# Optimization experiments

Measured on AMD Instinct MI355X. Metric: run time of the kernel, lower is better.

Reference implementation:

```python
import jax, jax.numpy as jnp
import numpy as np

G = 32               # sdf grid resolution (grid_size init default)
SCALE_FACTOR = 0.2   # forward default scale_factor
EPS = 1e-12


def setup_inputs() -> dict:
    key = jax.random.key(0)
    k1, k2 = jax.random.split(key)
    H, V, F = 2, 778, 1538  # two hands, MANO topology
    vertices = jax.random.normal(k1, (H, V, 3), dtype=jnp.float32)
    faces = jax.random.randint(k2, (F, 3), 0, V, dtype=jnp.int32)
    return {"vertices": vertices, "faces": faces}


def _sdiv(n, d):
    return n / jnp.where(jnp.abs(d) < EPS, EPS, d)


def _point_tri_dist2(p, a, b, c):
    # p: [P,1,3]; a,b,c: [1,F,3] -> squared distance [P,F] (Ericson closest-point)
    ab = b - a; ac = c - a; ap = p - a
    d1 = jnp.sum(ab * ap, -1); d2 = jnp.sum(ac * ap, -1)
    bp = p - b; d3 = jnp.sum(ab * bp, -1); d4 = jnp.sum(ac * bp, -1)
    cp = p - c; d5 = jnp.sum(ab * cp, -1); d6 = jnp.sum(ac * cp, -1)
    vc = d1 * d4 - d3 * d2
    vb = d5 * d2 - d1 * d6
    va = d3 * d6 - d5 * d4
    denom = va + vb + vc
    v_in = _sdiv(vb, denom); w_in = _sdiv(vc, denom)
    res = a + ab * v_in[..., None] + ac * w_in[..., None]  # face interior
    # edge BC
    cond = ((va <= 0) & ((d4 - d3) >= 0) & ((d5 - d6) >= 0))[..., None]
    w = _sdiv(d4 - d3, (d4 - d3) + (d5 - d6))[..., None]
    res = jnp.where(cond, b + (c - b) * w, res)
    # edge AC
    cond = ((vb <= 0) & (d2 >= 0) & (d6 <= 0))[..., None]
    w = _sdiv(d2, d2 - d6)[..., None]
    res = jnp.where(cond, a + ac * w, res)
    # edge AB
    cond = ((vc <= 0) & (d1 >= 0) & (d3 <= 0))[..., None]
    w = _sdiv(d1, d1 - d3)[..., None]
    res = jnp.where(cond, a + ab * w, res)
    # vertex regions (highest precedence)
    res = jnp.where(((d6 >= 0) & (d5 <= d6))[..., None], jnp.broadcast_to(c, res.shape), res)
    res = jnp.where(((d3 >= 0) & (d4 <= d3))[..., None], jnp.broadcast_to(b, res.shape), res)
    res = jnp.where(((d1 <= 0) & (d2 <= 0))[..., None], jnp.broadcast_to(a, res.shape), res)
    return jnp.sum((p - res) ** 2, -1)


def _inside(p, a, b, c):
    # parity of +x ray intersections (Moller-Trumbore with dir = (1,0,0))
    e1 = b - a; e2 = c - a
    det = e1[..., 1] * (-e2[..., 2]) + e1[..., 2] * e2[..., 1]  # dot(e1, cross(dir,e2))
    inv = _sdiv(1.0, det)
    s = p - a
    u = (s[..., 1] * (-e2[..., 2]) + s[..., 2] * e2[..., 1]) * inv
    q = jnp.cross(s, e1)
    v = q[..., 0] * inv                # dot(dir, q)
    t = jnp.sum(e2 * q, -1) * inv
    hit = (jnp.abs(det) > 1e-9) & (u >= 0) & (u <= 1) & (v >= 0) & (u + v <= 1) & (t > 0)
    return (jnp.sum(hit.astype(jnp.int32), axis=-1) % 2) == 1


def _sdf_grid(tri):
    # tri: [F,3,3] scaled triangles -> phi [G,G,G] laid out [z,y,x] (grid_sample DHW)
    a = tri[None, :, 0]; b = tri[None, :, 1]; c = tri[None, :, 2]
    lin = jnp.linspace(-1.0, 1.0, G, dtype=tri.dtype)
    zz, yy, xx = jnp.meshgrid(lin, lin, lin, indexing='ij')
    pts = jnp.stack([xx, yy, zz], -1).reshape(G, G * G, 3)  # chunk over z-slabs

    def slab(ps):
        p = ps[:, None, :]
        d2 = jnp.min(_point_tri_dist2(p, a, b, c), axis=1)
        ins = _inside(p, a, b, c)
        return jnp.where(ins, jnp.sqrt(jnp.maximum(d2, 0.0)), 0.0)

    return jax.lax.map(slab, pts).reshape(G, G, G)


def _trilinear(phi, coords):
    # grid_sample(align_corners=True, padding_mode='zeros'), coords [N,3] in xyz order
    g = G - 1
    f = (coords + 1.0) * 0.5 * g
    fx, fy, fz = f[:, 0], f[:, 1], f[:, 2]
    x0f = jnp.floor(fx); y0f = jnp.floor(fy); z0f = jnp.floor(fz)
    wx = fx - x0f; wy = fy - y0f; wz = fz - z0f
    x0 = x0f.astype(jnp.int32); y0 = y0f.astype(jnp.int32); z0 = z0f.astype(jnp.int32)

    def corner(zi, yi, xi, w):
        valid = (zi >= 0) & (zi <= g) & (yi >= 0) & (yi <= g) & (xi >= 0) & (xi <= g)
        val = phi[jnp.clip(zi, 0, g), jnp.clip(yi, 0, g), jnp.clip(xi, 0, g)]
        return jnp.where(valid, val, 0.0) * w

    out = (corner(z0, y0, x0, (1 - wz) * (1 - wy) * (1 - wx))
           + corner(z0, y0, x0 + 1, (1 - wz) * (1 - wy) * wx)
           + corner(z0, y0 + 1, x0, (1 - wz) * wy * (1 - wx))
           + corner(z0, y0 + 1, x0 + 1, (1 - wz) * wy * wx)
           + corner(z0 + 1, y0, x0, wz * (1 - wy) * (1 - wx))
           + corner(z0 + 1, y0, x0 + 1, wz * (1 - wy) * wx)
           + corner(z0 + 1, y0 + 1, x0, wz * wy * (1 - wx))
           + corner(z0 + 1, y0 + 1, x0 + 1, wz * wy * wx))
    return out


def reference(vertices, faces):
    H = vertices.shape[0]
    bmin = vertices.min(axis=1)   # [H,3]
    bmax = vertices.max(axis=1)
    center = jax.lax.stop_gradient(((bmin + bmax) * 0.5)[:, None, :])           # [H,1,3]
    scale = jax.lax.stop_gradient(
        ((1.0 + SCALE_FACTOR) * 0.5 * (bmax - bmin).max(-1))[:, None, None])    # [H,1,1]
    v_scaled = jax.lax.stop_gradient((vertices - center) / scale)
    tris = v_scaled[:, faces]                                                    # [H,F,3,3]
    phi = jax.lax.stop_gradient(jax.vmap(_sdf_grid)(tris))                       # [H,G,G,G]
    i = 1  # hardcoded loop 'for i in [1]' in the source
    coords = ((vertices - center[i][None]) / scale[i][None]).reshape(-1, 3)
    phi_val = _trilinear(phi[i], coords).reshape(H, -1)
    weights = jnp.ones((H, 1), dtype=vertices.dtype).at[i, 0].set(0.0)
    loss = jnp.sum(weights * phi_val) / (H ** 2)
    return loss
```

## Files before the change

kernel.cpp:

```cpp
#include <hip/hip_runtime.h>
#include <math.h>

#define NNODE 32768
#define NTHR  256
#define CH    256
#define MAXC  (CH + 63)

__device__ __forceinline__ float rguard(float d) {
    float dd = (fabsf(d) < 1e-12f) ? 1e-12f : d;
    return __builtin_amdgcn_rcpf(dd);
}

__device__ __forceinline__ void cell_of(float px, float py, float pz,
                                        int& x0, int& y0, int& z0,
                                        float& wx, float& wy, float& wz) {
#pragma clang fp contract(off)
    float fx = (px + 1.0f) * 0.5f * 31.0f;
    float fy = (py + 1.0f) * 0.5f * 31.0f;
    float fz = (pz + 1.0f) * 0.5f * 31.0f;
    float x0f = floorf(fx), y0f = floorf(fy), z0f = floorf(fz);
    wx = fx - x0f; wy = fy - y0f; wz = fz - z0f;
    x0 = (int)fmaxf(fminf(x0f, 33.0f), -2.0f);
    y0 = (int)fmaxf(fminf(y0f, 33.0f), -2.0f);
    z0 = (int)fmaxf(fminf(z0f, 33.0f), -2.0f);
}

__device__ __forceinline__ void bbox_of(const float* __restrict__ verts, int V,
                                        float& ocx, float& ocy, float& ocz,
                                        float& osc) {
#pragma clang fp contract(off)
    const float* v1 = verts + (size_t)V * 3;
    float mn[3] = {1e30f, 1e30f, 1e30f};
    float mx[3] = {-1e30f, -1e30f, -1e30f};
    for (int i = threadIdx.x; i < V; i += blockDim.x) {
        for (int c = 0; c < 3; ++c) {
            float val = v1[i * 3 + c];
            mn[c] = fminf(mn[c], val);
            mx[c] = fmaxf(mx[c], val);
        }
    }
    for (int off = 32; off >= 1; off >>= 1) {
        for (int c = 0; c < 3; ++c) {
            mn[c] = fminf(mn[c], __shfl_down(mn[c], off));
            mx[c] = fmaxf(mx[c], __shfl_down(mx[c], off));
        }
    }
    __shared__ float smn[16][3], smx[16][3];
    int wv = threadIdx.x >> 6, lane = threadIdx.x & 63;
    if (lane == 0)
        for (int c = 0; c < 3; ++c) { smn[wv][c] = mn[c]; smx[wv][c] = mx[c]; }
    __syncthreads();
    const int nw = (int)blockDim.x >> 6;
    float ext = -1e30f, cc[3];
    for (int c = 0; c < 3; ++c) {
        float lo = 1e30f, hi = -1e30f;
        for (int w = 0; w < nw; ++w) {
            lo = fminf(lo, smn[w][c]);
            hi = fmaxf(hi, smx[w][c]);
        }
        cc[c] = (lo + hi) * 0.5f;
        ext = fmaxf(ext, hi - lo);
    }
    ocx = cc[0]; ocy = cc[1]; ocz = cc[2];
    osc = (1.0f + 0.2f) * 0.5f * ext;
    __syncthreads();
}

__device__ __forceinline__ void tri_node(
        float ax, float ay, float az, float abx, float aby, float abz,
        float acx, float acy, float acz, float inv, float det,
        float dbb, float dbc, float dcc,
        float px, float py, float pz, float& mind2, int& h) {
    float apx = px - ax, apy = py - ay, apz = pz - az;
    {
#pragma clang fp contract(fast)
        float d1 = abx * apx + aby * apy + abz * apz;
        float d2 = acx * apx + acy * apy + acz * apz;
        float d3 = d1 - dbb;
        float d4 = d2 - dbc;
        float d5 = d1 - dbc;
        float d6 = d2 - dcc;
        float vc = d1 * d4 - d3 * d2;
        float vb = d5 * d2 - d1 * d6;
        float va = d3 * d6 - d5 * d4;
        float denom = va + vb + vc;
        float rd = rguard(denom);
        float v_in = vb * rd, w_in = vc * rd;
        float rx = ax + abx * v_in + acx * w_in;
        float ry = ay + aby * v_in + acy * w_in;
        float rz = az + abz * v_in + acz * w_in;
        if (va <= 0.0f && (d4 - d3) >= 0.0f && (d5 - d6) >= 0.0f) {
            float w2 = (d4 - d3) * rguard((d4 - d3) + (d5 - d6));
            rx = ax + abx + (acx - abx) * w2;
            ry = ay + aby + (acy - aby) * w2;
            rz = az + abz + (acz - abz) * w2;
        }
        if (vb <= 0.0f && d2 >= 0.0f && d6 <= 0.0f) {
            float w2 = d2 * rguard(d2 - d6);
            rx = ax + acx * w2; ry = ay + acy * w2; rz = az + acz * w2;
        }
        if (vc <= 0.0f && d1 >= 0.0f && d3 <= 0.0f) {
            float w2 = d1 * rguard(d1 - d3);
            rx = ax + abx * w2; ry = ay + aby * w2; rz = az + abz * w2;
        }
        if (d6 >= 0.0f && d5 <= d6) { rx = ax + acx; ry = ay + acy; rz = az + acz; }
        if (d3 >= 0.0f && d4 <= d3) { rx = ax + abx; ry = ay + aby; rz = az + abz; }
        if (d1 <= 0.0f && d2 <= 0.0f) { rx = ax; ry = ay; rz = az; }
        float ddx = px - rx, ddy = py - ry, ddz = pz - rz;
        mind2 = fminf(mind2, ddx * ddx + ddy * ddy + ddz * ddz);
    }
    {
#pragma clang fp contract(off)
        float u = (apy * (-acz) + apz * acy) * inv;
        float qx = apy * abz - apz * aby;
        float qy = apz * abx - apx * abz;
        float qz = apx * aby - apy * abx;
        float v = qx * inv;
        float tt = (acx * qx + acy * qy + acz * qz) * inv;
        h += (fabsf(det) > 1e-9f && u >= 0.0f && u <= 1.0f && v >= 0.0f &&
              (u + v) <= 1.0f && tt > 0.0f) ? 1 : 0;
    }
}

__global__ void __launch_bounds__(NTHR) k_setup(
        const float* __restrict__ verts, const int* __restrict__ faces,
        float* __restrict__ tri, unsigned int* __restrict__ d2b,
        int* __restrict__ hits, int* __restrict__ cnt, int* __restrict__ list,
        int V, int F) {
    float cx0, cy0, cz0, sc;
    bbox_of(verts, V, cx0, cy0, cz0, sc);
    const int b = (int)blockIdx.x, tid = threadIdx.x;

    for (int t = b * NTHR + tid; t < NNODE; t += (int)gridDim.x * NTHR) {
        d2b[t] = 0xFFFFFFFFu;
        hits[t] = 0;
    }

    if (b == 0) {
        __shared__ unsigned bm[NNODE / 32];
        __shared__ int scnt[NTHR];
        for (int k = 0; k < 4; ++k) bm[tid * 4 + k] = 0u;
        __syncthreads();
        for (int i = tid; i < V; i += NTHR) {
#pragma clang fp contract(off)
            float px = (verts[i * 3 + 0] - cx0) / sc;
            float py = (verts[i * 3 + 1] - cy0) / sc;
            float pz = (verts[i * 3 + 2] - cz0) / sc;
            int x0, y0, z0; float wx, wy, wz;
            cell_of(px, py, pz, x0, y0, z0, wx, wy, wz);
            for (int k = 0; k < 8; ++k) {
                int zi = z0 + ((k >> 2) & 1), yi = y0 + ((k >> 1) & 1),
                    xi = x0 + (k & 1);
                if ((unsigned)zi < 32u && (unsigned)yi < 32u && (unsigned)xi < 32u) {
                    int node = (zi * 32 + yi) * 32 + xi;
                    atomicOr(&bm[node >> 5], 1u << (node & 31));
                }
            }
        }
        __syncthreads();
        unsigned w0 = bm[tid * 4 + 0], w1 = bm[tid * 4 + 1],
                 w2 = bm[tid * 4 + 2], w3 = bm[tid * 4 + 3];
        int c = __popc(w0) + __popc(w1) + __popc(w2) + __popc(w3);
        scnt[tid] = c;
        __syncthreads();
        for (int off = 1; off < NTHR; off <<= 1) {
            int v_ = (tid >= off) ? scnt[tid - off] : 0;
            __syncthreads();
            scnt[tid] += v_;
            __syncthreads();
        }
        if (tid == NTHR - 1) cnt[0] = scnt[NTHR - 1];
        int off = scnt[tid] - c;
        unsigned wsv[4] = {w0, w1, w2, w3};
        for (int k = 0; k < 4; ++k) {
            unsigned w = wsv[k];
            int basebit = (tid * 4 + k) * 32;
            while (w) {
                int bb = __ffs(w) - 1;
                list[off++] = basebit + bb;
                w &= w - 1;
            }
        }
    } else {
        int f = (b - 1) * NTHR + tid;
        if (f < F) {
#pragma clang fp contract(off)
            const float* v1 = verts + (size_t)V * 3;
            int i0 = faces[f * 3 + 0], i1 = faces[f * 3 + 1], i2 = faces[f * 3 + 2];
            float ax = (v1[i0 * 3 + 0] - cx0) / sc, ay = (v1[i0 * 3 + 1] - cy0) / sc,
                  az = (v1[i0 * 3 + 2] - cz0) / sc;
            float bx = (v1[i1 * 3 + 0] - cx0) / sc, by = (v1[i1 * 3 + 1] - cy0) / sc,
                  bz = (v1[i1 * 3 + 2] - cz0) / sc;
            float cx = (v1[i2 * 3 + 0] - cx0) / sc, cy = (v1[i2 * 3 + 1] - cy0) / sc,
                  cz = (v1[i2 * 3 + 2] - cz0) / sc;
            float abx = bx - ax, aby = by - ay, abz = bz - az;
            float acx = cx - ax, acy = cy - ay, acz = cz - az;
            float det = aby * (-acz) + abz * acy;
            float dd = (fabsf(det) < 1e-12f) ? 1e-12f : det;
            float inv = 1.0f / dd;
            float* r = tri + (size_t)f * 16;
            r[0] = ax;  r[1] = ay;  r[2] = az;
            r[3] = abx; r[4] = aby; r[5] = abz;
            r[6] = acx; r[7] = acy; r[8] = acz;
            r[9] = inv; r[10] = det;
            r[11] = abx * abx + aby * aby + abz * abz;
            r[12] = abx * acx + aby * acy + abz * acz;
            r[13] = acx * acx + acy * acy + acz * acz;
            r[14] = 0.0f; r[15] = 0.0f;
        }
    }
}

__global__ void __launch_bounds__(NTHR) k_main(
        const float* __restrict__ tri, const int* __restrict__ list,
        const int* __restrict__ cnt, unsigned int* __restrict__ d2b,
        int* __restrict__ hits, int F, int nch) {
    const int n = cnt[0];
    const int group = (int)blockIdx.x / nch;
    if (group * 4 >= n) return;
    const int c = (int)blockIdx.x - group * nch;
    const int cbase = c * CH;
    const int tn = (c == nch - 1) ? (F - cbase) : CH;

    __shared__ float s[14][MAXC];
    const int tid = threadIdx.x, lane = tid & 63;
    for (int j = tid; j < tn; j += NTHR) {
        const float4* g = (const float4*)(tri + (size_t)(cbase + j) * 16);
        float4 r0 = g[0], r1 = g[1], r2 = g[2], r3 = g[3];
        s[0][j] = r0.x;  s[1][j] = r0.y;  s[2][j] = r0.z;  s[3][j] = r0.w;
        s[4][j] = r1.x;  s[5][j] = r1.y;  s[6][j] = r1.z;  s[7][j] = r1.w;
        s[8][j] = r2.x;  s[9][j] = r2.y;  s[10][j] = r2.z; s[11][j] = r2.w;
        s[12][j] = r3.x; s[13][j] = r3.y;
    }
    __syncthreads();

    const int idx = group * 4 + (tid >> 6);
    const int node = (idx < n) ? list[idx] : -1;
    float px = 0, py = 0, pz = 0;
    if (node >= 0) {
#pragma clang fp contract(off)
        px = (float)((double)(node & 31) * (2.0 / 31.0) - 1.0);
        py = (float)((double)((node >> 5) & 31) * (2.0 / 31.0) - 1.0);
        pz = (float)((double)(node >> 10) * (2.0 / 31.0) - 1.0);
    }
    float m = 1e30f;
    int h = 0;
    if (node >= 0) {
        for (int mi = 0; mi * 64 < tn; ++mi) {
            int j = lane + mi * 64;
            if (j < tn) {
                tri_node(s[0][j], s[1][j], s[2][j], s[3][j], s[4][j], s[5][j],
                         s[6][j], s[7][j], s[8][j], s[9][j], s[10][j],
                         s[11][j], s[12][j], s[13][j], px, py, pz, m, h);
            }
        }
    }
    for (int off = 32; off >= 1; off >>= 1) {
        m = fminf(m, __shfl_xor(m, off));
        h += __shfl_xor(h, off);
    }
    if (lane == 0 && node >= 0) {
        atomicMin(d2b + node, __float_as_uint(m));
        atomicAdd(hits + node, h);
    }
}

__global__ void k_sum(const float* __restrict__ verts,
                      const unsigned int* __restrict__ d2b, const int* __restrict__ hits,
                      float* __restrict__ out, int V) {
    float cx, cy, cz, sc;
    bbox_of(verts, V, cx, cy, cz, sc);
    {
#pragma clang fp contract(off)
        __shared__ float sm[1024];
        const int tid = threadIdx.x;
        float val = 0.0f;
        for (int i = tid; i < V; i += 1024) {
            float px = (verts[i * 3 + 0] - cx) / sc;
            float py = (verts[i * 3 + 1] - cy) / sc;
            float pz = (verts[i * 3 + 2] - cz) / sc;
            int x0, y0, z0; float wx, wy, wz;
            cell_of(px, py, pz, x0, y0, z0, wx, wy, wz);
            auto corner = [&](int zi, int yi, int xi, float w) -> float {
#pragma clang fp contract(off)
                bool valid = (zi >= 0) && (zi <= 31) && (yi >= 0) && (yi <= 31) &&
                             (xi >= 0) && (xi <= 31);
                int zc = min(max(zi, 0), 31);
                int yc = min(max(yi, 0), 31);
                int xc = min(max(xi, 0), 31);
                int idx = (zc * 32 + yc) * 32 + xc;
                float vv = (hits[idx] & 1)
                               ? sqrtf(fmaxf(__uint_as_float(d2b[idx]), 0.0f))
                               : 0.0f;
                return valid ? vv * w : 0.0f;
            };
            val += corner(z0, y0, x0, (1.0f - wz) * (1.0f - wy) * (1.0f - wx))
                 + corner(z0, y0, x0 + 1, (1.0f - wz) * (1.0f - wy) * wx)
                 + corner(z0, y0 + 1, x0, (1.0f - wz) * wy * (1.0f - wx))
                 + corner(z0, y0 + 1, x0 + 1, (1.0f - wz) * wy * wx)
                 + corner(z0 + 1, y0, x0, wz * (1.0f - wy) * (1.0f - wx))
                 + corner(z0 + 1, y0, x0 + 1, wz * (1.0f - wy) * wx)
                 + corner(z0 + 1, y0 + 1, x0, wz * wy * (1.0f - wx))
                 + corner(z0 + 1, y0 + 1, x0 + 1, wz * wy * wx);
        }
        sm[tid] = val;
        __syncthreads();
        for (int ss = 512; ss >= 1; ss >>= 1) {
            if (tid < ss) sm[tid] += sm[tid + ss];
            __syncthreads();
        }
        if (tid == 0) out[0] = sm[0] * 0.25f;
    }
}

extern "C" void kernel_launch(void* const* d_in, const int* in_sizes, int n_in,
                              void* d_out, int out_size, void* d_ws, size_t ws_size,
                              hipStream_t stream) {
    const float* verts = (const float*)d_in[0];
    const int* faces = (const int*)d_in[1];
    float* out = (float*)d_out;
    float* ws = (float*)d_ws;

    int V = in_sizes[0] / 6;
    int F = in_sizes[1] / 3;

    float* tri = ws;
    unsigned int* d2b = (unsigned int*)(tri + 16 * (size_t)F);
    int* hits = (int*)(d2b + NNODE);
    int* cnt = hits + NNODE;
    int* list = cnt + 1;

    int nrec = (F + NTHR - 1) / NTHR;
    int nch = F / CH;
    int rem = F - nch * CH;
    if (nch == 0 || rem >= 64) nch += (rem > 0 ? 1 : 0);
    if (nch == 0) nch = 1;

    int nmax = 8 * V; if (nmax > NNODE) nmax = NNODE;
    int nblk_main = ((nmax + 3) / 4) * nch;

    k_setup<<<1 + nrec, NTHR, 0, stream>>>(verts, faces, tri, d2b, hits, cnt, list,
                                           V, F);
    k_main<<<nblk_main, NTHR, 0, stream>>>(tri, list, cnt, d2b, hits, F, nch);
    k_sum<<<1, 1024, 0, stream>>>(verts, d2b, hits, out, V);
}
```

Baseline: 44.69 us.

## Widen setup block, init only touched nodes, split final sum across blocks

The setup kernel now runs with 1024 threads per block, so the node bitmap is handled one word per thread, and it resets d2b/hits only for nodes in the active list instead of clearing all 32768 entries. The final reduction is spread over 8 blocks that combine partial sums through a fixed-point 64-bit atomic and a last-block-done counter. The goal is to remove the full-grid clear and the single-block serial sum. The fixed-point conversion and the counter protocol change rounding slightly, and correctness depends on the memory ordering between the atomics.

```diff
diff --git a/kernel.cpp b/kernel.cpp
--- a/kernel.cpp
+++ b/kernel.cpp
@@ -3,8 +3,10 @@
 
 #define NNODE 32768
 #define NTHR  256
+#define STHR  1024
 #define CH    256
 #define MAXC  (CH + 63)
+#define SUMB  8
 
 __device__ __forceinline__ float rguard(float d) {
     float dd = (fabsf(d) < 1e-12f) ? 1e-12f : d;
@@ -122,26 +124,22 @@
     }
 }
 
-__global__ void __launch_bounds__(NTHR) k_setup(
+__global__ void __launch_bounds__(STHR) k_setup(
         const float* __restrict__ verts, const int* __restrict__ faces,
         float* __restrict__ tri, unsigned int* __restrict__ d2b,
-        int* __restrict__ hits, int* __restrict__ cnt, int* __restrict__ list,
-        int V, int F) {
+        int* __restrict__ hits, int* __restrict__ cnt,
+        unsigned long long* __restrict__ acc, int* __restrict__ done2,
+        int* __restrict__ list, int V, int F) {
     float cx0, cy0, cz0, sc;
     bbox_of(verts, V, cx0, cy0, cz0, sc);
     const int b = (int)blockIdx.x, tid = threadIdx.x;
 
-    for (int t = b * NTHR + tid; t < NNODE; t += (int)gridDim.x * NTHR) {
-        d2b[t] = 0xFFFFFFFFu;
-        hits[t] = 0;
-    }
-
     if (b == 0) {
         __shared__ unsigned bm[NNODE / 32];
-        __shared__ int scnt[NTHR];
-        for (int k = 0; k < 4; ++k) bm[tid * 4 + k] = 0u;
-        __syncthreads();
-        for (int i = tid; i < V; i += NTHR) {
+        __shared__ int scnt[STHR];
+        bm[tid] = 0u;
+        __syncthreads();
+        for (int i = tid; i < V; i += STHR) {
 #pragma clang fp contract(off)
             float px = (verts[i * 3 + 0] - cx0) / sc;
             float py = (verts[i * 3 + 1] - cy0) / sc;
@@ -158,31 +156,34 @@
             }
         }
         __syncthreads();
-        unsigned w0 = bm[tid * 4 + 0], w1 = bm[tid * 4 + 1],
-                 w2 = bm[tid * 4 + 2], w3 = bm[tid * 4 + 3];
-        int c = __popc(w0) + __popc(w1) + __popc(w2) + __popc(w3);
+        unsigned w0 = bm[tid];
+        int c = __popc(w0);
         scnt[tid] = c;
         __syncthreads();
-        for (int off = 1; off < NTHR; off <<= 1) {
+        for (int off = 1; off < STHR; off <<= 1) {
             int v_ = (tid >= off) ? scnt[tid - off] : 0;
             __syncthreads();
             scnt[tid] += v_;
             __syncthreads();
         }
-        if (tid == NTHR - 1) cnt[0] = scnt[NTHR - 1];
+        int total = scnt[STHR - 1];
+        if (tid == STHR - 1) cnt[0] = total;
         int off = scnt[tid] - c;
-        unsigned wsv[4] = {w0, w1, w2, w3};
-        for (int k = 0; k < 4; ++k) {
-            unsigned w = wsv[k];
-            int basebit = (tid * 4 + k) * 32;
-            while (w) {
-                int bb = __ffs(w) - 1;
-                list[off++] = basebit + bb;
-                w &= w - 1;
-            }
-        }
+        int basebit = tid * 32;
+        while (w0) {
+            int bb = __ffs(w0) - 1;
+            list[off++] = basebit + bb;
+            w0 &= w0 - 1;
+        }
+        __syncthreads();
+        for (int t = tid; t < total; t += STHR) {
+            int nd = list[t];
+            d2b[nd] = 0xFFFFFFFFu;
+            hits[nd] = 0;
+        }
+        if (tid == 0) { acc[0] = 0ull; done2[0] = 0; }
     } else {
-        int f = (b - 1) * NTHR + tid;
+        int f = (b - 1) * STHR + tid;
         if (f < F) {
 #pragma clang fp contract(off)
             const float* v1 = verts + (size_t)V * 3;
@@ -265,17 +266,16 @@
     }
 }
 
-__global__ void k_sum(const float* __restrict__ verts,
-                      const unsigned int* __restrict__ d2b, const int* __restrict__ hits,
-                      float* __restrict__ out, int V) {
+__global__ void __launch_bounds__(NTHR) k_sum(
+        const float* __restrict__ verts, const unsigned int* __restrict__ d2b,
+        const int* __restrict__ hits, unsigned long long* __restrict__ acc,
+        int* __restrict__ done2, float* __restrict__ out, int V) {
     float cx, cy, cz, sc;
     bbox_of(verts, V, cx, cy, cz, sc);
+    float val = 0.0f;
     {
 #pragma clang fp contract(off)
-        __shared__ float sm[1024];
-        const int tid = threadIdx.x;
-        float val = 0.0f;
-        for (int i = tid; i < V; i += 1024) {
+        for (int i = (int)blockIdx.x * NTHR + threadIdx.x; i < V; i += SUMB * NTHR) {
             float px = (verts[i * 3 + 0] - cx) / sc;
             float py = (verts[i * 3 + 1] - cy) / sc;
             float pz = (verts[i * 3 + 2] - cz) / sc;
@@ -303,13 +303,25 @@
                  + corner(z0 + 1, y0 + 1, x0, wz * wy * (1.0f - wx))
                  + corner(z0 + 1, y0 + 1, x0 + 1, wz * wy * wx);
         }
-        sm[tid] = val;
-        __syncthreads();
-        for (int ss = 512; ss >= 1; ss >>= 1) {
-            if (tid < ss) sm[tid] += sm[tid + ss];
-            __syncthreads();
-        }
-        if (tid == 0) out[0] = sm[0] * 0.25f;
+    }
+    __shared__ float sm[NTHR];
+    const int tid = threadIdx.x;
+    sm[tid] = val;
+    __syncthreads();
+    for (int ss = NTHR / 2; ss >= 1; ss >>= 1) {
+        if (tid < ss) sm[tid] += sm[tid + ss];
+        __syncthreads();
+    }
+    if (tid == 0) {
+        unsigned long long fx =
+            (unsigned long long)((double)sm[0] * 4294967296.0);
+        atomicAdd(acc, fx);
+        asm volatile("s_waitcnt vmcnt(0)");
+        int prev = atomicAdd(done2, 1);
+        if (prev == SUMB - 1) {
+            unsigned long long tot = atomicAdd(acc, 0ull);
+            out[0] = (float)((double)tot / 4294967296.0 * 0.25);
+        }
     }
 }
 
@@ -324,23 +336,25 @@
     int V = in_sizes[0] / 6;
     int F = in_sizes[1] / 3;
 
-    float* tri = ws;
+    unsigned long long* acc = (unsigned long long*)ws;
+    int* done2 = (int*)(ws + 2);
+    int* cnt = (int*)(ws + 3);
+    float* tri = ws + 4;
     unsigned int* d2b = (unsigned int*)(tri + 16 * (size_t)F);
     int* hits = (int*)(d2b + NNODE);
-    int* cnt = hits + NNODE;
-    int* list = cnt + 1;
-
-    int nrec = (F + NTHR - 1) / NTHR;
+    int* list = hits + NNODE;
+
     int nch = F / CH;
     int rem = F - nch * CH;
     if (nch == 0 || rem >= 64) nch += (rem > 0 ? 1 : 0);
     if (nch == 0) nch = 1;
 
+    int nrec = (F + STHR - 1) / STHR;
     int nmax = 8 * V; if (nmax > NNODE) nmax = NNODE;
     int nblk_main = ((nmax + 3) / 4) * nch;
 
-    k_setup<<<1 + nrec, NTHR, 0, stream>>>(verts, faces, tri, d2b, hits, cnt, list,
-                                           V, F);
+    k_setup<<<1 + nrec, STHR, 0, stream>>>(verts, faces, tri, d2b, hits, cnt, acc,
+                                           done2, list, V, F);
     k_main<<<nblk_main, NTHR, 0, stream>>>(tri, list, cnt, d2b, hits, F, nch);
-    k_sum<<<1, 1024, 0, stream>>>(verts, d2b, hits, out, V);
-}
+    k_sum<<<SUMB, NTHR, 0, stream>>>(verts, d2b, hits, acc, done2, out, V);
+}
```

New measurement: 44.34 us. Within noise of the previous version (-0.8%).
